# Optimization experiments

Measured on AMD Instinct MI355X. Metric: run time of the kernel, lower is better.

The kernel has to match this reference:

```python
import jax, jax.numpy as jnp
import numpy as np

B, T, D = 4, 2048, 1024


def setup_inputs() -> dict:
    key = jax.random.key(0)
    ks = jax.random.split(key, 14)
    s = 0.02
    return {
        "x": jax.random.normal(ks[0], (B, T, D), dtype=jnp.float32),
        "time_decay": jax.random.normal(ks[1], (D,), dtype=jnp.float32) * 0.1,
        "tm_k": jax.random.uniform(ks[2], (D,), dtype=jnp.float32),
        "tm_v": jax.random.uniform(ks[3], (D,), dtype=jnp.float32),
        "tm_r": jax.random.uniform(ks[4], (D,), dtype=jnp.float32),
        "Wk": jax.random.normal(ks[5], (D, D), dtype=jnp.float32) * s,
        "Wv": jax.random.normal(ks[6], (D, D), dtype=jnp.float32) * s,
        "Wr": jax.random.normal(ks[7], (D, D), dtype=jnp.float32) * s,
        "Wo": jax.random.normal(ks[8], (D, D), dtype=jnp.float32) * s,
        "cm_k": jax.random.uniform(ks[9], (D,), dtype=jnp.float32),
        "cm_r": jax.random.uniform(ks[10], (D,), dtype=jnp.float32),
        "Wck": jax.random.normal(ks[11], (D, 4 * D), dtype=jnp.float32) * s,
        "Wcv": jax.random.normal(ks[12], (4 * D, D), dtype=jnp.float32) * s,
        "Wcr": jax.random.normal(ks[13], (D, D), dtype=jnp.float32) * s,
    }


def _shift(x):
    # token shift: prepend zero state (initial last_x), drop last token
    return jnp.concatenate([jnp.zeros_like(x[:, :1]), x[:, :-1]], axis=1)


def reference(x, time_decay, tm_k, tm_v, tm_r, Wk, Wv, Wr, Wo,
              cm_k, cm_r, Wck, Wcv, Wcr):
    # ---- time mixing (WKV recurrence) ----
    shifted = _shift(x)
    xk = x * tm_k + shifted * (1.0 - tm_k)
    xv = x * tm_v + shifted * (1.0 - tm_v)
    xr = x * tm_r + shifted * (1.0 - tm_r)
    k = xk @ Wk            # (B,T,D)
    v = xv @ Wv
    r = jax.nn.sigmoid(xr @ Wr)
    ew = jnp.exp(-jnp.exp(time_decay))  # exp(w), w = -exp(time_decay)

    def step(carry, kv):
        num, den = carry
        kt, vt = kv
        ek = jnp.exp(kt)
        num = ew * num + ek * vt
        den = ew * den + ek
        return (num, den), num / (den + 1e-6)

    init = (jnp.zeros((B, D), x.dtype), jnp.zeros((B, D), x.dtype))
    _, wkv_t = jax.lax.scan(step, init, (jnp.swapaxes(k, 0, 1), jnp.swapaxes(v, 0, 1)))
    wkv = jnp.swapaxes(wkv_t, 0, 1)  # (B,T,D)
    x = x + (r * wkv) @ Wo

    # ---- channel mixing (gated FFN, squared ReLU) ----
    shifted2 = _shift(x)
    xk2 = x * cm_k + shifted2 * (1.0 - cm_k)
    xr2 = x * cm_r + shifted2 * (1.0 - cm_r)
    kh = jnp.square(jax.nn.relu(xk2 @ Wck))  # (B,T,4D)
    v2 = kh @ Wcv
    r2 = jax.nn.sigmoid(xr2 @ Wcr)
    return x + r2 * v2
```

## Files before the change

kernel.cpp:

```cpp
#include <hip/hip_runtime.h>
#include <hip/hip_bf16.h>
#include <math.h>

#define BATCH 4
#define TLEN  2048
#define DIM   1024
#define NROWS (BATCH*TLEN)
#define HDIM  (4*DIM)

typedef __hip_bfloat16 bf16;
typedef __attribute__((ext_vector_type(8))) short   shortx8;
typedef __attribute__((ext_vector_type(4))) float   floatx4;

__device__ __forceinline__ unsigned short f2bf(float f) {
    bf16 h = __float2bfloat16(f);
    return __builtin_bit_cast(unsigned short, h);
}

__device__ __forceinline__ void async16(const void* g, void* l) {
    __builtin_amdgcn_global_load_lds((const __attribute__((address_space(1))) void*)g,
                                     (__attribute__((address_space(3))) void*)l, 16, 0, 0);
}

enum { EP_NONE=0, EP_SIGMOID=1, EP_ADD=2, EP_SQRELU=3, EP_FINAL=4 };

template<int MODE, typename OutT>
__global__ __launch_bounds__(256)
void mfma_gemm(const bf16* __restrict__ A, const bf16* __restrict__ Bt,
               OutT* __restrict__ C,
               const float* __restrict__ addv, const bf16* __restrict__ mulv,
               int M, int N, int K)
{
    __shared__ bf16 As[128*64];
    __shared__ bf16 Bs[128*64];
    const int tid  = threadIdx.x;
    const int lane = tid & 63;
    const int wave = tid >> 6;
    const int wm   = (wave >> 1) * 64;
    const int wn   = (wave & 1) * 64;
    const size_t m0 = (size_t)blockIdx.x * 128;
    const size_t n0 = (size_t)blockIdx.y * 128;

    const int r0 = tid >> 3;
    const int kg = (tid & 7) ^ (r0 & 7);
    const int c0 = kg * 8;
    const bf16* ag[4];
    const bf16* bg[4];
    #pragma unroll
    for (int j = 0; j < 4; ++j) {
        ag[j] = A  + (m0 + r0 + j*32) * K + c0;
        bg[j] = Bt + (n0 + r0 + j*32) * K + c0;
    }

    floatx4 acc[4][4] = {};

    const int mrow = lane & 15;
    const int kqg  = lane >> 4;
    const int kx   = mrow & 7;

    for (int k0 = 0; k0 < K; k0 += 64) {
        #pragma unroll
        for (int j = 0; j < 4; ++j) async16(ag[j] + k0, As + (tid + j*256) * 8);
        #pragma unroll
        for (int j = 0; j < 4; ++j) async16(bg[j] + k0, Bs + (tid + j*256) * 8);
        __syncthreads();

        #pragma unroll
        for (int ks = 0; ks < 2; ++ks) {
            const int kcol = ((ks*4 + kqg) ^ kx) << 3;
            shortx8 af[4], bfr[4];
            #pragma unroll
            for (int i = 0; i < 4; ++i) {
                af[i]  = *(const shortx8*)(As + (wm + i*16 + mrow)*64 + kcol);
                bfr[i] = *(const shortx8*)(Bs + (wn + i*16 + mrow)*64 + kcol);
            }
            #pragma unroll
            for (int mi = 0; mi < 4; ++mi)
                #pragma unroll
                for (int ni = 0; ni < 4; ++ni)
                    acc[mi][ni] = __builtin_amdgcn_mfma_f32_16x16x32_bf16(
                                      af[mi], bfr[ni], acc[mi][ni], 0, 0, 0);
        }
        __syncthreads();
    }

    const int crow = (lane >> 4) * 4;
    const int ccol = lane & 15;
    #pragma unroll
    for (int mi = 0; mi < 4; ++mi) {
        #pragma unroll
        for (int ni = 0; ni < 4; ++ni) {
            #pragma unroll
            for (int r = 0; r < 4; ++r) {
                size_t row = m0 + wm + mi*16 + crow + r;
                size_t col = n0 + wn + ni*16 + ccol;
                size_t off = row * N + col;
                float v = acc[mi][ni][r];
                if (MODE == EP_SIGMOID)      v = 1.0f / (1.0f + __expf(-v));
                else if (MODE == EP_ADD)     v = addv[off] + v;
                else if (MODE == EP_SQRELU)  { float t = fmaxf(v, 0.0f); v = t * t; }
                else if (MODE == EP_FINAL)   v = addv[off] + __bfloat162float(mulv[off]) * v;
                if (sizeof(OutT) == 2) *(unsigned short*)(C + off) = f2bf(v);
                else                   *(float*)(C + off) = v;
            }
        }
    }
}

struct GDesc { const bf16* A; const bf16* Bt; bf16* C; int N; int K; int mode; int ntiles; };
struct GArgs { GDesc d[3]; };

__global__ __launch_bounds__(256)
void mfma_gemm_multi(GArgs args)
{
    int by = blockIdx.y, di = 0;
    while (by >= args.d[di].ntiles) { by -= args.d[di].ntiles; ++di; }
    const bf16* A  = args.d[di].A;
    const bf16* Bt = args.d[di].Bt;
    bf16*       C  = args.d[di].C;
    const int   N  = args.d[di].N;
    const int   K  = args.d[di].K;
    const int   mode = args.d[di].mode;

    __shared__ bf16 As[128*64];
    __shared__ bf16 Bs[128*64];
    const int tid  = threadIdx.x;
    const int lane = tid & 63;
    const int wave = tid >> 6;
    const int wm   = (wave >> 1) * 64;
    const int wn   = (wave & 1) * 64;
    const size_t m0 = (size_t)blockIdx.x * 128;
    const size_t n0 = (size_t)by * 128;

    const int r0 = tid >> 3;
    const int kg = (tid & 7) ^ (r0 & 7);
    const int c0 = kg * 8;
    const bf16* ag[4];
    const bf16* bg[4];
    #pragma unroll
    for (int j = 0; j < 4; ++j) {
        ag[j] = A  + (m0 + r0 + j*32) * K + c0;
        bg[j] = Bt + (n0 + r0 + j*32) * K + c0;
    }

    floatx4 acc[4][4] = {};

    const int mrow = lane & 15;
    const int kqg  = lane >> 4;
    const int kx   = mrow & 7;

    for (int k0 = 0; k0 < K; k0 += 64) {
        #pragma unroll
        for (int j = 0; j < 4; ++j) async16(ag[j] + k0, As + (tid + j*256) * 8);
        #pragma unroll
        for (int j = 0; j < 4; ++j) async16(bg[j] + k0, Bs + (tid + j*256) * 8);
        __syncthreads();

        #pragma unroll
        for (int ks = 0; ks < 2; ++ks) {
            const int kcol = ((ks*4 + kqg) ^ kx) << 3;
            shortx8 af[4], bfr[4];
            #pragma unroll
            for (int i = 0; i < 4; ++i) {
                af[i]  = *(const shortx8*)(As + (wm + i*16 + mrow)*64 + kcol);
                bfr[i] = *(const shortx8*)(Bs + (wn + i*16 + mrow)*64 + kcol);
            }
            #pragma unroll
            for (int mi = 0; mi < 4; ++mi)
                #pragma unroll
                for (int ni = 0; ni < 4; ++ni)
                    acc[mi][ni] = __builtin_amdgcn_mfma_f32_16x16x32_bf16(
                                      af[mi], bfr[ni], acc[mi][ni], 0, 0, 0);
        }
        __syncthreads();
    }

    const int crow = (lane >> 4) * 4;
    const int ccol = lane & 15;
    #pragma unroll
    for (int mi = 0; mi < 4; ++mi) {
        #pragma unroll
        for (int ni = 0; ni < 4; ++ni) {
            #pragma unroll
            for (int r = 0; r < 4; ++r) {
                size_t row = m0 + wm + mi*16 + crow + r;
                size_t col = n0 + wn + ni*16 + ccol;
                float v = acc[mi][ni][r];
                if (mode == EP_SIGMOID)     v = 1.0f / (1.0f + __expf(-v));
                else if (mode == EP_SQRELU) { float t = fmaxf(v, 0.0f); v = t * t; }
                *(unsigned short*)(C + row * N + col) = f2bf(v);
            }
        }
    }
}

struct TDesc { const float* in; bf16* out; int K; int N; int tiles; int tx; };
struct PrepArgs {
    TDesc t[7];
    int ttotal;
    const float4 *x, *mk, *mv, *mr;
    ushort4 *ok, *ov, *orr;
};

__global__ __launch_bounds__(256)
void prep_kernel(PrepArgs a)
{
    int blk = blockIdx.x;
    if (blk < a.ttotal) {
        int t = blk, di = 0;
        while (t >= a.t[di].tiles) { t -= a.t[di].tiles; ++di; }
        const float* in  = a.t[di].in;
        bf16*        out = a.t[di].out;
        const int K = a.t[di].K, N = a.t[di].N, tx = a.t[di].tx;
        const int bx = t % tx, by = t / tx;
        __shared__ float tile[32][33];
        const int kt = by * 32, nt = bx * 32;
        #pragma unroll
        for (int i = threadIdx.y; i < 32; i += 8)
            tile[i][threadIdx.x] = in[(size_t)(kt + i) * N + nt + threadIdx.x];
        __syncthreads();
        #pragma unroll
        for (int i = threadIdx.y; i < 32; i += 8)
            out[(size_t)(nt + i) * K + kt + threadIdx.x] =
                __float2bfloat16(tile[threadIdx.x][i]);
    } else {
        const int D4 = DIM / 4;
        int tid = threadIdx.y * 32 + threadIdx.x;
        int e   = (blk - a.ttotal) * 256 + tid;
        int d4  = e & (D4 - 1);
        int t   = (e >> 8) & (TLEN - 1);
        float4 xc = a.x[e];
        float4 sh = make_float4(0.f, 0.f, 0.f, 0.f);
        if (t > 0) sh = a.x[e - D4];
        float4 mk = a.mk[d4], mv = a.mv[d4], mr = a.mr[d4];
        ushort4 u;
        u.x=f2bf(xc.x*mk.x+sh.x*(1.f-mk.x)); u.y=f2bf(xc.y*mk.y+sh.y*(1.f-mk.y));
        u.z=f2bf(xc.z*mk.z+sh.z*(1.f-mk.z)); u.w=f2bf(xc.w*mk.w+sh.w*(1.f-mk.w));
        a.ok[e]=u;
        u.x=f2bf(xc.x*mv.x+sh.x*(1.f-mv.x)); u.y=f2bf(xc.y*mv.y+sh.y*(1.f-mv.y));
        u.z=f2bf(xc.z*mv.z+sh.z*(1.f-mv.z)); u.w=f2bf(xc.w*mv.w+sh.w*(1.f-mv.w));
        a.ov[e]=u;
        u.x=f2bf(xc.x*mr.x+sh.x*(1.f-mr.x)); u.y=f2bf(xc.y*mr.y+sh.y*(1.f-mr.y));
        u.z=f2bf(xc.z*mr.z+sh.z*(1.f-mr.z)); u.w=f2bf(xc.w*mr.w+sh.w*(1.f-mr.w));
        a.orr[e]=u;
    }
}

__global__ __launch_bounds__(256)
void mix2_kernel(const float4* __restrict__ x,
                 const float4* __restrict__ mk, const float4* __restrict__ mr,
                 ushort4* __restrict__ ok, ushort4* __restrict__ orr)
{
    const int D4 = DIM / 4;
    int e   = blockIdx.x * 256 + threadIdx.x;
    int d4  = e & (D4 - 1);
    int t   = (e >> 8) & (TLEN - 1);
    float4 xc = x[e];
    float4 sh = make_float4(0.f, 0.f, 0.f, 0.f);
    if (t > 0) sh = x[e - D4];
    float4 a = mk[d4], c = mr[d4];
    ushort4 u;
    u.x=f2bf(xc.x*a.x+sh.x*(1.f-a.x)); u.y=f2bf(xc.y*a.y+sh.y*(1.f-a.y));
    u.z=f2bf(xc.z*a.z+sh.z*(1.f-a.z)); u.w=f2bf(xc.w*a.w+sh.w*(1.f-a.w));
    ok[e]=u;
    u.x=f2bf(xc.x*c.x+sh.x*(1.f-c.x)); u.y=f2bf(xc.y*c.y+sh.y*(1.f-c.y));
    u.z=f2bf(xc.z*c.z+sh.z*(1.f-c.z)); u.w=f2bf(xc.w*c.w+sh.w*(1.f-c.w));
    orr[e]=u;
}

#define WKV_CHUNK 64
#define WKV_WARM  64
__global__ __launch_bounds__(256)
void wkv_kernel(const bf16* __restrict__ K, const bf16* __restrict__ V,
                const bf16* __restrict__ R, const float* __restrict__ td,
                bf16* __restrict__ out)
{
    int d     = blockIdx.x * 256 + threadIdx.x;
    int chunk = blockIdx.y;
    int b     = blockIdx.z;
    int start = chunk * WKV_CHUNK;
    int t0    = start - WKV_WARM; if (t0 < 0) t0 = 0;

    float ew = __expf(-__expf(td[d]));
    float num = 0.f, den = 0.f;
    size_t base = ((size_t)b * TLEN) * DIM + d;

    for (int t = t0; t < start; ++t) {
        size_t idx = base + (size_t)t * DIM;
        float ek = __expf(__bfloat162float(K[idx]));
        num = ew * num + ek * __bfloat162float(V[idx]);
        den = ew * den + ek;
    }
    for (int t = start; t < start + WKV_CHUNK; ++t) {
        size_t idx = base + (size_t)t * DIM;
        float ek = __expf(__bfloat162float(K[idx]));
        num = ew * num + ek * __bfloat162float(V[idx]);
        den = ew * den + ek;
        out[idx] = __float2bfloat16(__bfloat162float(R[idx]) * (num / (den + 1e-6f)));
    }
}

extern "C" void kernel_launch(void* const* d_in, const int* in_sizes, int n_in,
                              void* d_out, int out_size, void* d_ws, size_t ws_size,
                              hipStream_t stream)
{
    const float* x   = (const float*)d_in[0];
    const float* td  = (const float*)d_in[1];
    const float* tmk = (const float*)d_in[2];
    const float* tmv = (const float*)d_in[3];
    const float* tmr = (const float*)d_in[4];
    const float* Wk  = (const float*)d_in[5];
    const float* Wv  = (const float*)d_in[6];
    const float* Wr  = (const float*)d_in[7];
    const float* Wo  = (const float*)d_in[8];
    const float* cmk = (const float*)d_in[9];
    const float* cmr = (const float*)d_in[10];
    const float* Wck = (const float*)d_in[11];
    const float* Wcv = (const float*)d_in[12];
    const float* Wcr = (const float*)d_in[13];
    float* out = (float*)d_out;

    char* ws = (char*)d_ws;
    const size_t MB = 1024 * 1024;
    bf16*  Wk_t  = (bf16*)(ws +   0*MB);
    bf16*  Wv_t  = (bf16*)(ws +   2*MB);
    bf16*  Wr_t  = (bf16*)(ws +   4*MB);
    bf16*  Wo_t  = (bf16*)(ws +   6*MB);
    bf16*  Wcr_t = (bf16*)(ws +   8*MB);
    bf16*  Wck_t = (bf16*)(ws +  10*MB);
    bf16*  Wcv_t = (bf16*)(ws +  18*MB);
    float* f0    = (float*)(ws + 26*MB);
    bf16*  bA    = (bf16*)(ws +  58*MB);
    bf16*  bB    = (bf16*)(ws +  74*MB);
    bf16*  bC    = (bf16*)(ws +  90*MB);
    bf16*  bD    = (bf16*)(ws + 106*MB);
    bf16*  bE    = (bf16*)(ws + 122*MB);
    bf16*  bF    = (bf16*)(ws + 138*MB);
    bf16*  kh    = bA;

    const dim3 blk(256);

    {
        PrepArgs pa;
        const float* src[7] = {Wk, Wv, Wr, Wo, Wcr, Wck, Wcv};
        bf16*        dst[7] = {Wk_t, Wv_t, Wr_t, Wo_t, Wcr_t, Wck_t, Wcv_t};
        int          kk[7]  = {DIM, DIM, DIM, DIM, DIM, DIM, HDIM};
        int          nn[7]  = {DIM, DIM, DIM, DIM, DIM, HDIM, DIM};
        int total = 0;
        for (int i = 0; i < 7; ++i) {
            int tx = nn[i] / 32, ty = kk[i] / 32;
            pa.t[i] = {src[i], dst[i], kk[i], nn[i], tx * ty, tx};
            total += tx * ty;
        }
        pa.ttotal = total;
        pa.x  = (const float4*)x;
        pa.mk = (const float4*)tmk; pa.mv = (const float4*)tmv; pa.mr = (const float4*)tmr;
        pa.ok = (ushort4*)bA; pa.ov = (ushort4*)bB; pa.orr = (ushort4*)bC;
        const int mixBlocks = NROWS * DIM / 4 / 256;
        prep_kernel<<<dim3(total + mixBlocks), dim3(32, 8), 0, stream>>>(pa);
    }

    {
        GArgs ga;
        ga.d[0] = {bA, Wk_t, bD, DIM, DIM, EP_NONE,    8};
        ga.d[1] = {bB, Wv_t, bE, DIM, DIM, EP_NONE,    8};
        ga.d[2] = {bC, Wr_t, bF, DIM, DIM, EP_SIGMOID, 8};
        mfma_gemm_multi<<<dim3(NROWS/128, 24), blk, 0, stream>>>(ga);
    }

    dim3 wkvGrid(DIM / 256, TLEN / WKV_CHUNK, BATCH);
    wkv_kernel<<<wkvGrid, blk, 0, stream>>>(bD, bE, bF, td, bF);

    mfma_gemm<EP_ADD, float><<<dim3(NROWS/128, DIM/128), blk, 0, stream>>>(
        bF, Wo_t, f0, x, nullptr, NROWS, DIM, DIM);

    mix2_kernel<<<dim3(NROWS * DIM / 4 / 256), blk, 0, stream>>>(
        (const float4*)f0, (const float4*)cmk, (const float4*)cmr,
        (ushort4*)bE, (ushort4*)bA);

    mfma_gemm<EP_SIGMOID, bf16><<<dim3(NROWS/128, DIM/128), blk, 0, stream>>>(
        bA, Wcr_t, bF, nullptr, nullptr, NROWS, DIM, DIM);

    mfma_gemm<EP_SQRELU, bf16><<<dim3(NROWS/128, HDIM/128), blk, 0, stream>>>(
        bE, Wck_t, kh, nullptr, nullptr, NROWS, HDIM, DIM);

    mfma_gemm<EP_FINAL, float><<<dim3(NROWS/128, DIM/128), blk, 0, stream>>>(
        kh, Wcv_t, out, f0, bF, NROWS, DIM, HDIM);
}
```

Baseline: 499.7 us.

## Replace GEMMs with 128x256 tile, 512-thread, 5-stage async-LDS pipelined kernel

Replaces the single-buffered 128x128 MFMA GEMM with a 128x256 tile kernel run by 8 waves. It uses a 5-slot LDS ring with K-step 32 and explicit vmcnt waits, so global-to-LDS loads overlap MFMA compute instead of stalling on a syncthreads per iteration. It also adds a new XOR swizzle, s_setprio around the MFMA bursts, and a block-index remap for L2 locality. The change aims to hide memory latency and raise MFMA utilisation. In exchange it uses more LDS and registers per block, and the hand-tuned waitcnt scheme is fragile.

```diff
diff --git a/kernel.cpp b/kernel.cpp
--- a/kernel.cpp
+++ b/kernel.cpp
@@ -24,174 +24,182 @@
 
 enum { EP_NONE=0, EP_SIGMOID=1, EP_ADD=2, EP_SQRELU=3, EP_FINAL=4 };
 
-template<int MODE, typename OutT>
-__global__ __launch_bounds__(256)
-void mfma_gemm(const bf16* __restrict__ A, const bf16* __restrict__ Bt,
-               OutT* __restrict__ C,
-               const float* __restrict__ addv, const bf16* __restrict__ mulv,
-               int M, int N, int K)
-{
-    __shared__ bf16 As[128*64];
-    __shared__ bf16 Bs[128*64];
-    const int tid  = threadIdx.x;
+#define G_REGB   24576
+#define G_ABYTES 8192
+#define G_NSH    (5*12288)
+
+__device__ __forceinline__ void gemm_core(
+    const bf16* __restrict__ A, const bf16* __restrict__ Bt, const int K,
+    const size_t m0, const size_t n0, short* lds, floatx4 (&acc)[4][4])
+{
+    const int tid = threadIdx.x;
+    char* ldsc = (char*)lds;
+
+    const int rA = tid >> 2;
+    const int kA = ((tid & 3) ^ ((rA >> 1) & 3)) << 3;
+    const bf16* pA  = A  + (size_t)(m0 + rA) * K + kA;
+    const int s1  = 512 + tid;
+    const int rB1 = s1 >> 2;
+    const int kB1 = ((s1 & 3) ^ ((rB1 >> 1) & 3)) << 3;
+    const bf16* pB0 = Bt + (size_t)(n0 + rA)  * K + kA;
+    const bf16* pB1 = Bt + (size_t)(n0 + rB1) * K + kB1;
+    char* dA  = ldsc + tid * 16;
+    char* dB0 = ldsc + G_ABYTES + tid * 16;
+    char* dB1 = ldsc + G_ABYTES + 8192 + tid * 16;
+
     const int lane = tid & 63;
     const int wave = tid >> 6;
-    const int wm   = (wave >> 1) * 64;
-    const int wn   = (wave & 1) * 64;
-    const size_t m0 = (size_t)blockIdx.x * 128;
-    const size_t n0 = (size_t)blockIdx.y * 128;
-
-    const int r0 = tid >> 3;
-    const int kg = (tid & 7) ^ (r0 & 7);
-    const int c0 = kg * 8;
-    const bf16* ag[4];
-    const bf16* bg[4];
+    const int wm = (wave >> 2) * 64;
+    const int wn = (wave & 3) * 64;
+    const int lr = lane & 15, kq = lane >> 4;
+    int offA[4], offB[4];
     #pragma unroll
-    for (int j = 0; j < 4; ++j) {
-        ag[j] = A  + (m0 + r0 + j*32) * K + c0;
-        bg[j] = Bt + (n0 + r0 + j*32) * K + c0;
-    }
-
+    for (int i = 0; i < 4; ++i) {
+        const int ra = wm + i*16 + lr;
+        offA[i] = ra*64 + ((kq ^ ((ra>>1)&3)) << 4);
+        const int rb = wn + i*16 + lr;
+        offB[i] = G_ABYTES + rb*64 + ((kq ^ ((rb>>1)&3)) << 4);
+    }
+
+    const int P = K >> 5;
+
+    auto stage = [&](int sl, int reg) {
+        const int rB = reg * G_REGB;
+        const int ko = sl << 5;
+        async16(pA  + ko, dA  + rB);
+        async16(pB0 + ko, dB0 + rB);
+        async16(pB1 + ko, dB1 + rB);
+    };
+    auto compute = [&](int reg) {
+        const char* rb = ldsc + reg * G_REGB;
+        shortx8 af[4], bfr[4];
+        #pragma unroll
+        for (int i = 0; i < 4; ++i) af[i]  = *(const shortx8*)(rb + offA[i]);
+        #pragma unroll
+        for (int i = 0; i < 4; ++i) bfr[i] = *(const shortx8*)(rb + offB[i]);
+        __builtin_amdgcn_s_setprio(1);
+        #pragma unroll
+        for (int mi = 0; mi < 4; ++mi)
+            #pragma unroll
+            for (int ni = 0; ni < 4; ++ni)
+                acc[mi][ni] = __builtin_amdgcn_mfma_f32_16x16x32_bf16(
+                                  af[mi], bfr[ni], acc[mi][ni], 0, 0, 0);
+        __builtin_amdgcn_s_setprio(0);
+    };
+
+    stage(0,0); stage(1,1); stage(2,2); stage(3,3);
+    asm volatile("s_waitcnt vmcnt(9)" ::: "memory");
+    __builtin_amdgcn_s_barrier();
+    __builtin_amdgcn_sched_barrier(0);
+
+    int cur = 0, sreg = 4;
+    for (int q = 0; q < P - 4; ++q) {
+        stage(q + 4, sreg);
+        compute(cur);
+        asm volatile("s_waitcnt vmcnt(9)" ::: "memory");
+        __builtin_amdgcn_s_barrier();
+        __builtin_amdgcn_sched_barrier(0);
+        sreg = cur;
+        cur  = (cur == 4) ? 0 : cur + 1;
+    }
+    compute(cur); cur = (cur == 4) ? 0 : cur + 1;
+    asm volatile("s_waitcnt vmcnt(6)" ::: "memory");
+    __builtin_amdgcn_s_barrier();
+    __builtin_amdgcn_sched_barrier(0);
+    compute(cur); cur = (cur == 4) ? 0 : cur + 1;
+    asm volatile("s_waitcnt vmcnt(3)" ::: "memory");
+    __builtin_amdgcn_s_barrier();
+    __builtin_amdgcn_sched_barrier(0);
+    compute(cur); cur = (cur == 4) ? 0 : cur + 1;
+    asm volatile("s_waitcnt vmcnt(0)" ::: "memory");
+    __builtin_amdgcn_s_barrier();
+    __builtin_amdgcn_sched_barrier(0);
+    compute(cur);
+}
+
+template<int MODE, typename OutT>
+__device__ __forceinline__ void epilogue(
+    floatx4 (&acc)[4][4], OutT* __restrict__ C,
+    const float* __restrict__ addv, const bf16* __restrict__ mulv,
+    const size_t m0, const size_t n0, const int N)
+{
+    const int tid = threadIdx.x;
+    const int lane = tid & 63, wave = tid >> 6;
+    const size_t r0 = m0 + (size_t)(wave >> 2) * 64 + ((lane >> 4) << 2);
+    const size_t c0 = n0 + (size_t)(wave & 3) * 64 + (lane & 15);
+    #pragma unroll
+    for (int mi = 0; mi < 4; ++mi)
+      #pragma unroll
+      for (int ni = 0; ni < 4; ++ni)
+        #pragma unroll
+        for (int r = 0; r < 4; ++r) {
+            const size_t off = (r0 + mi*16 + r) * N + c0 + ni*16;
+            float v = acc[mi][ni][r];
+            if (MODE == EP_SIGMOID)      v = 1.0f / (1.0f + __expf(-v));
+            else if (MODE == EP_ADD)     v = addv[off] + v;
+            else if (MODE == EP_SQRELU)  { float t = fmaxf(v, 0.0f); v = t * t; }
+            else if (MODE == EP_FINAL)   v = addv[off] + __bfloat162float(mulv[off]) * v;
+            if (sizeof(OutT) == 2) *(unsigned short*)(C + off) = f2bf(v);
+            else                   *(float*)(C + off) = v;
+        }
+}
+
+template<int MODE, typename OutT>
+__global__ __launch_bounds__(512, 2)
+void gemm256(const bf16* __restrict__ A, const bf16* __restrict__ Bt,
+             OutT* __restrict__ C,
+             const float* __restrict__ addv, const bf16* __restrict__ mulv,
+             int N, int K)
+{
+    __shared__ __align__(16) short lds[G_NSH];
+    const int nwg  = gridDim.x * gridDim.y;
+    const int orig = blockIdx.y * gridDim.x + blockIdx.x;
+    const int wg   = (orig & 7) * (nwg >> 3) + (orig >> 3);
+    const int bx   = wg % gridDim.x;
+    const int by   = wg / gridDim.x;
+    const size_t m0 = (size_t)bx * 128;
+    const size_t n0 = (size_t)by * 256;
     floatx4 acc[4][4] = {};
-
-    const int mrow = lane & 15;
-    const int kqg  = lane >> 4;
-    const int kx   = mrow & 7;
-
-    for (int k0 = 0; k0 < K; k0 += 64) {
-        #pragma unroll
-        for (int j = 0; j < 4; ++j) async16(ag[j] + k0, As + (tid + j*256) * 8);
-        #pragma unroll
-        for (int j = 0; j < 4; ++j) async16(bg[j] + k0, Bs + (tid + j*256) * 8);
-        __syncthreads();
-
-        #pragma unroll
-        for (int ks = 0; ks < 2; ++ks) {
-            const int kcol = ((ks*4 + kqg) ^ kx) << 3;
-            shortx8 af[4], bfr[4];
-            #pragma unroll
-            for (int i = 0; i < 4; ++i) {
-                af[i]  = *(const shortx8*)(As + (wm + i*16 + mrow)*64 + kcol);
-                bfr[i] = *(const shortx8*)(Bs + (wn + i*16 + mrow)*64 + kcol);
-            }
-            #pragma unroll
-            for (int mi = 0; mi < 4; ++mi)
-                #pragma unroll
-                for (int ni = 0; ni < 4; ++ni)
-                    acc[mi][ni] = __builtin_amdgcn_mfma_f32_16x16x32_bf16(
-                                      af[mi], bfr[ni], acc[mi][ni], 0, 0, 0);
+    gemm_core(A, Bt, K, m0, n0, lds, acc);
+    epilogue<MODE, OutT>(acc, C, addv, mulv, m0, n0, N);
+}
+
+struct GDesc { const bf16* A; const bf16* Bt; bf16* C; int mode; };
+struct GArgs { GDesc d[3]; };
+
+__global__ __launch_bounds__(512, 2)
+void gemm256_multi(GArgs args)
+{
+    __shared__ __align__(16) short lds[G_NSH];
+    const int nwg  = gridDim.x * gridDim.y;
+    const int orig = blockIdx.y * gridDim.x + blockIdx.x;
+    const int wg   = (orig & 7) * (nwg >> 3) + (orig >> 3);
+    const int bx   = wg % gridDim.x;
+    const int byg  = wg / gridDim.x;
+    const int di   = byg >> 2;
+    const int by   = byg & 3;
+    const GDesc d  = args.d[di];
+    const size_t m0 = (size_t)bx * 128;
+    const size_t n0 = (size_t)by * 256;
+    floatx4 acc[4][4] = {};
+    gemm_core(d.A, d.Bt, DIM, m0, n0, lds, acc);
+
+    const int tid = threadIdx.x;
+    const int lane = tid & 63, wave = tid >> 6;
+    const size_t r0 = m0 + (size_t)(wave >> 2) * 64 + ((lane >> 4) << 2);
+    const size_t c0 = n0 + (size_t)(wave & 3) * 64 + (lane & 15);
+    const bool sig = (d.mode == EP_SIGMOID);
+    #pragma unroll
+    for (int mi = 0; mi < 4; ++mi)
+      #pragma unroll
+      for (int ni = 0; ni < 4; ++ni)
+        #pragma unroll
+        for (int r = 0; r < 4; ++r) {
+            const size_t off = (r0 + mi*16 + r) * DIM + c0 + ni*16;
+            float v = acc[mi][ni][r];
+            if (sig) v = 1.0f / (1.0f + __expf(-v));
+            *(unsigned short*)(d.C + off) = f2bf(v);
         }
-        __syncthreads();
-    }
-
-    const int crow = (lane >> 4) * 4;
-    const int ccol = lane & 15;
-    #pragma unroll
-    for (int mi = 0; mi < 4; ++mi) {
-        #pragma unroll
-        for (int ni = 0; ni < 4; ++ni) {
-            #pragma unroll
-            for (int r = 0; r < 4; ++r) {
-                size_t row = m0 + wm + mi*16 + crow + r;
-                size_t col = n0 + wn + ni*16 + ccol;
-                size_t off = row * N + col;
-                float v = acc[mi][ni][r];
-                if (MODE == EP_SIGMOID)      v = 1.0f / (1.0f + __expf(-v));
-                else if (MODE == EP_ADD)     v = addv[off] + v;
-                else if (MODE == EP_SQRELU)  { float t = fmaxf(v, 0.0f); v = t * t; }
-                else if (MODE == EP_FINAL)   v = addv[off] + __bfloat162float(mulv[off]) * v;
-                if (sizeof(OutT) == 2) *(unsigned short*)(C + off) = f2bf(v);
-                else                   *(float*)(C + off) = v;
-            }
-        }
-    }
-}
-
-struct GDesc { const bf16* A; const bf16* Bt; bf16* C; int N; int K; int mode; int ntiles; };
-struct GArgs { GDesc d[3]; };
-
-__global__ __launch_bounds__(256)
-void mfma_gemm_multi(GArgs args)
-{
-    int by = blockIdx.y, di = 0;
-    while (by >= args.d[di].ntiles) { by -= args.d[di].ntiles; ++di; }
-    const bf16* A  = args.d[di].A;
-    const bf16* Bt = args.d[di].Bt;
-    bf16*       C  = args.d[di].C;
-    const int   N  = args.d[di].N;
-    const int   K  = args.d[di].K;
-    const int   mode = args.d[di].mode;
-
-    __shared__ bf16 As[128*64];
-    __shared__ bf16 Bs[128*64];
-    const int tid  = threadIdx.x;
-    const int lane = tid & 63;
-    const int wave = tid >> 6;
-    const int wm   = (wave >> 1) * 64;
-    const int wn   = (wave & 1) * 64;
-    const size_t m0 = (size_t)blockIdx.x * 128;
-    const size_t n0 = (size_t)by * 128;
-
-    const int r0 = tid >> 3;
-    const int kg = (tid & 7) ^ (r0 & 7);
-    const int c0 = kg * 8;
-    const bf16* ag[4];
-    const bf16* bg[4];
-    #pragma unroll
-    for (int j = 0; j < 4; ++j) {
-        ag[j] = A  + (m0 + r0 + j*32) * K + c0;
-        bg[j] = Bt + (n0 + r0 + j*32) * K + c0;
-    }
-
-    floatx4 acc[4][4] = {};
-
-    const int mrow = lane & 15;
-    const int kqg  = lane >> 4;
-    const int kx   = mrow & 7;
-
-    for (int k0 = 0; k0 < K; k0 += 64) {
-        #pragma unroll
-        for (int j = 0; j < 4; ++j) async16(ag[j] + k0, As + (tid + j*256) * 8);
-        #pragma unroll
-        for (int j = 0; j < 4; ++j) async16(bg[j] + k0, Bs + (tid + j*256) * 8);
-        __syncthreads();
-
-        #pragma unroll
-        for (int ks = 0; ks < 2; ++ks) {
-            const int kcol = ((ks*4 + kqg) ^ kx) << 3;
-            shortx8 af[4], bfr[4];
-            #pragma unroll
-            for (int i = 0; i < 4; ++i) {
-                af[i]  = *(const shortx8*)(As + (wm + i*16 + mrow)*64 + kcol);
-                bfr[i] = *(const shortx8*)(Bs + (wn + i*16 + mrow)*64 + kcol);
-            }
-            #pragma unroll
-            for (int mi = 0; mi < 4; ++mi)
-                #pragma unroll
-                for (int ni = 0; ni < 4; ++ni)
-                    acc[mi][ni] = __builtin_amdgcn_mfma_f32_16x16x32_bf16(
-                                      af[mi], bfr[ni], acc[mi][ni], 0, 0, 0);
-        }
-        __syncthreads();
-    }
-
-    const int crow = (lane >> 4) * 4;
-    const int ccol = lane & 15;
-    #pragma unroll
-    for (int mi = 0; mi < 4; ++mi) {
-        #pragma unroll
-        for (int ni = 0; ni < 4; ++ni) {
-            #pragma unroll
-            for (int r = 0; r < 4; ++r) {
-                size_t row = m0 + wm + mi*16 + crow + r;
-                size_t col = n0 + wn + ni*16 + ccol;
-                float v = acc[mi][ni][r];
-                if (mode == EP_SIGMOID)     v = 1.0f / (1.0f + __expf(-v));
-                else if (mode == EP_SQRELU) { float t = fmaxf(v, 0.0f); v = t * t; }
-                *(unsigned short*)(C + row * N + col) = f2bf(v);
-            }
-        }
-    }
 }
 
 struct TDesc { const float* in; bf16* out; int K; int N; int tiles; int tx; };
@@ -339,6 +347,7 @@
     bf16*  kh    = bA;
 
     const dim3 blk(256);
+    const dim3 gblk(512);
 
     {
         PrepArgs pa;
@@ -362,28 +371,28 @@
 
     {
         GArgs ga;
-        ga.d[0] = {bA, Wk_t, bD, DIM, DIM, EP_NONE,    8};
-        ga.d[1] = {bB, Wv_t, bE, DIM, DIM, EP_NONE,    8};
-        ga.d[2] = {bC, Wr_t, bF, DIM, DIM, EP_SIGMOID, 8};
-        mfma_gemm_multi<<<dim3(NROWS/128, 24), blk, 0, stream>>>(ga);
+        ga.d[0] = {bA, Wk_t, bD, EP_NONE};
+        ga.d[1] = {bB, Wv_t, bE, EP_NONE};
+        ga.d[2] = {bC, Wr_t, bF, EP_SIGMOID};
+        gemm256_multi<<<dim3(NROWS/128, 12), gblk, 0, stream>>>(ga);
     }
 
     dim3 wkvGrid(DIM / 256, TLEN / WKV_CHUNK, BATCH);
     wkv_kernel<<<wkvGrid, blk, 0, stream>>>(bD, bE, bF, td, bF);
 
-    mfma_gemm<EP_ADD, float><<<dim3(NROWS/128, DIM/128), blk, 0, stream>>>(
-        bF, Wo_t, f0, x, nullptr, NROWS, DIM, DIM);
+    gemm256<EP_ADD, float><<<dim3(NROWS/128, DIM/256), gblk, 0, stream>>>(
+        bF, Wo_t, f0, x, nullptr, DIM, DIM);
 
     mix2_kernel<<<dim3(NROWS * DIM / 4 / 256), blk, 0, stream>>>(
         (const float4*)f0, (const float4*)cmk, (const float4*)cmr,
         (ushort4*)bE, (ushort4*)bA);
 
-    mfma_gemm<EP_SIGMOID, bf16><<<dim3(NROWS/128, DIM/128), blk, 0, stream>>>(
-        bA, Wcr_t, bF, nullptr, nullptr, NROWS, DIM, DIM);
-
-    mfma_gemm<EP_SQRELU, bf16><<<dim3(NROWS/128, HDIM/128), blk, 0, stream>>>(
-        bE, Wck_t, kh, nullptr, nullptr, NROWS, HDIM, DIM);
-
-    mfma_gemm<EP_FINAL, float><<<dim3(NROWS/128, DIM/128), blk, 0, stream>>>(
-        kh, Wcv_t, out, f0, bF, NROWS, DIM, HDIM);
-}
+    gemm256<EP_SIGMOID, bf16><<<dim3(NROWS/128, DIM/256), gblk, 0, stream>>>(
+        bA, Wcr_t, bF, nullptr, nullptr, DIM, DIM);
+
+    gemm256<EP_SQRELU, bf16><<<dim3(NROWS/128, HDIM/256), gblk, 0, stream>>>(
+        bE, Wck_t, kh, nullptr, nullptr, HDIM, DIM);
+
+    gemm256<EP_FINAL, float><<<dim3(NROWS/128, DIM/256), gblk, 0, stream>>>(
+        kh, Wcv_t, out, f0, bF, DIM, HDIM);
+}
```

New measurement: 489.6 us. 1.02x faster.
